# Optimization experiments

Hardware: AMD Instinct MI355X
Metric: run time of the kernel (lower is better)

## Reference

```python
import jax, jax.numpy as jnp
import numpy as np

N = 100000
E = 6400000
NT_DIM = 8
HID = 32


def setup_inputs() -> dict:
    key = jax.random.key(0)
    k1, k2, k3, k4, k5, k6, k7 = jax.random.split(key, 7)
    nt_emb = jax.random.normal(k1, (N, NT_DIM), dtype=jnp.float32)
    edge_index = jax.random.randint(k2, (2, E), 0, N, dtype=jnp.int64)
    lm_mask = jax.random.uniform(k3, (N,), dtype=jnp.float32)
    fan_in1 = 2 * NT_DIM + 2
    lim1 = 1.0 / np.sqrt(fan_in1)
    W1 = jax.random.uniform(k4, (fan_in1, HID), minval=-lim1, maxval=lim1, dtype=jnp.float32)
    b1 = jax.random.uniform(k5, (HID,), minval=-lim1, maxval=lim1, dtype=jnp.float32)
    lim2 = 1.0 / np.sqrt(HID)
    W2 = jax.random.uniform(k6, (HID, 1), minval=-lim2, maxval=lim2, dtype=jnp.float32)
    b2 = jax.random.uniform(k7, (1,), minval=-lim2, maxval=lim2, dtype=jnp.float32)
    return {"nt_emb": nt_emb, "edge_index": edge_index, "lm_mask": lm_mask,
            "W1": W1, "b1": b1, "W2": W2, "b2": b2}


def reference(nt_emb, edge_index, lm_mask, W1, b1, W2, b2):
    s, d = edge_index[0], edge_index[1]
    # [E, 2*nt_dim + 2] edge features: src emb, dst emb, src mask, dst mask
    feat = jnp.concatenate(
        [nt_emb[s], nt_emb[d], lm_mask[s][:, None], lm_mask[d][:, None]], axis=-1)
    h = jax.nn.relu(feat @ W1 + b1)          # [E, hid]
    out = jax.nn.sigmoid(h @ W2 + b2)        # [E, 1]
    return out[:, 0]                         # [E]
```

## Files before the change

### kernel.cpp

```cpp
#include <hip/hip_runtime.h>
#include <hip/hip_bf16.h>

typedef short short8 __attribute__((ext_vector_type(8)));
typedef float floatx4 __attribute__((ext_vector_type(4)));
typedef float floatx16 __attribute__((ext_vector_type(16)));

#define HID 32
#define NTD 8
#define FAN_IN 18

__device__ __forceinline__ short f2bf(float f) {
    union { float f; unsigned u; } v; v.f = f;
    unsigned r = v.u + 0x7fffu + ((v.u >> 16) & 1u);
    return (short)(r >> 16);
}

__device__ __forceinline__ float fast_sigmoid(float x) {
    float e = __builtin_amdgcn_exp2f(x * -1.44269504f);
    return __builtin_amdgcn_rcpf(1.0f + e);
}

__global__ void build_table(const float* __restrict__ emb,
                            const float* __restrict__ mask,
                            short* __restrict__ T, int N) {
    int n = blockIdx.x * blockDim.x + threadIdx.x;
    if (n >= N) return;
    const float4* p = (const float4*)(emb + (size_t)n * NTD);
    float4 lo = p[0], hi = p[1];
    short8 a, b;
    a[0] = f2bf(lo.x); a[1] = f2bf(lo.y); a[2] = f2bf(lo.z); a[3] = f2bf(lo.w);
    a[4] = f2bf(hi.x); a[5] = f2bf(hi.y); a[6] = f2bf(hi.z); a[7] = f2bf(hi.w);
    b[0] = f2bf(mask[n]); b[1] = (short)0x3F80;
    b[2] = b[3] = b[4] = b[5] = b[6] = b[7] = 0;
    short8* row = (short8*)(T + (size_t)n * 16);
    row[0] = a; row[1] = b;
}

struct IdxQ { unsigned sA, dA, sB, dB; };

template <int ESZ>
__device__ __forceinline__ IdxQ load_idx(const char* __restrict__ sBase,
                                         const char* __restrict__ dBase,
                                         unsigned grp, unsigned nGroups,
                                         unsigned E, unsigned c) {
    unsigned g = grp < nGroups ? grp : nGroups - 1u;
    unsigned eA = g * 64u + c;
    unsigned eB = eA + 32u;
    if (eA >= E) eA = E - 1u;
    if (eB >= E) eB = E - 1u;
    IdxQ q;
    q.sA = *(const unsigned*)(sBase + eA * (unsigned)ESZ);
    q.dA = *(const unsigned*)(dBase + eA * (unsigned)ESZ);
    q.sB = *(const unsigned*)(sBase + eB * (unsigned)ESZ);
    q.dB = *(const unsigned*)(dBase + eB * (unsigned)ESZ);
    return q;
}

__device__ __forceinline__ short8 g16(const char* __restrict__ Tc, unsigned idx, unsigned hoff) {
    return *(const short8*)(Tc + (idx * 32u + hoff));
}

template <int ESZ>
__device__ void run32(const char* __restrict__ ei,
                      const char* __restrict__ Tc,
                      float* __restrict__ out, unsigned E,
                      short8 as, short8 ad, const float* __restrict__ w2r, float bias2,
                      unsigned waveId, unsigned nWaves, int h, int c, int lane) {
    const unsigned nGroups = (E + 63u) >> 6;
    const char* sBase = ei;
    const char* dBase = ei + (size_t)E * ESZ;
    const unsigned hoff = (unsigned)h * 16u;

    if (waveId >= nGroups) return;

    unsigned cur = waveId;
    const unsigned stride2 = 2u * nWaves;

    IdxQ i0 = load_idx<ESZ>(sBase, dBase, cur, nGroups, E, (unsigned)c);
    short8 bsA = g16(Tc, i0.sA, hoff);
    short8 bdA = g16(Tc, i0.dA, hoff);
    short8 bsB = g16(Tc, i0.sB, hoff);
    short8 bdB = g16(Tc, i0.dB, hoff);
    IdxQ i1 = load_idx<ESZ>(sBase, dBase, cur + nWaves, nGroups, E, (unsigned)c);

    while (true) {
        short8 nsA = g16(Tc, i1.sA, hoff);
        short8 ndA = g16(Tc, i1.dA, hoff);
        short8 nsB = g16(Tc, i1.sB, hoff);
        short8 ndB = g16(Tc, i1.dB, hoff);
        IdxQ i2 = load_idx<ESZ>(sBase, dBase, cur + stride2, nGroups, E, (unsigned)c);

        floatx16 accA = {0.f,0.f,0.f,0.f,0.f,0.f,0.f,0.f,0.f,0.f,0.f,0.f,0.f,0.f,0.f,0.f};
        floatx16 accB = accA;
        accA = __builtin_amdgcn_mfma_f32_32x32x16_bf16(as, bsA, accA, 0, 0, 0);
        accB = __builtin_amdgcn_mfma_f32_32x32x16_bf16(as, bsB, accB, 0, 0, 0);
        accA = __builtin_amdgcn_mfma_f32_32x32x16_bf16(ad, bdA, accA, 0, 0, 0);
        accB = __builtin_amdgcn_mfma_f32_32x32x16_bf16(ad, bdB, accB, 0, 0, 0);

        float pA0 = 0.f, pA1 = 0.f, pB0 = 0.f, pB1 = 0.f;
        #pragma unroll
        for (int q = 0; q < 16; q += 2) {
            pA0 += fmaxf(accA[q],     0.f) * w2r[q];
            pA1 += fmaxf(accA[q + 1], 0.f) * w2r[q + 1];
            pB0 += fmaxf(accB[q],     0.f) * w2r[q];
            pB1 += fmaxf(accB[q + 1], 0.f) * w2r[q + 1];
        }
        float pA = pA0 + pA1;
        float pB = pB0 + pB1;
        pA += __shfl_xor(pA, 32, 64);
        pB += __shfl_xor(pB, 32, 64);
        float vA = fast_sigmoid(pA + bias2);
        float vB = fast_sigmoid(pB + bias2);

        float v = (h == 0) ? vA : vB;
        unsigned base = cur << 6;
        unsigned e = base + (unsigned)lane;
        if (base + 64u <= E) {
            out[e] = v;
        } else if (e < E) {
            out[e] = v;
        }

        cur += nWaves;
        if (cur >= nGroups) break;
        bsA = nsA; bdA = ndA; bsB = nsB; bdB = ndB;
        i1 = i2;
    }
}

__global__ __launch_bounds__(256, 4) void lg_table_kernel(
    const char* __restrict__ ei_bytes,
    const short* __restrict__ T,
    const float* __restrict__ W1,
    const float* __restrict__ b1,
    const float* __restrict__ W2,
    const float* __restrict__ b2,
    float* __restrict__ out,
    long long E)
{
    const int lane = threadIdx.x & 63;
    const int waveInBlock = threadIdx.x >> 6;
    const unsigned waveId = (unsigned)(blockIdx.x * (blockDim.x >> 6) + waveInBlock);
    const unsigned nWaves = (unsigned)(gridDim.x * (blockDim.x >> 6));

    const int* ei32 = (const int*)ei_bytes;
    int probe = ei32[2 * lane + 1];
    unsigned long long nz = __ballot(probe != 0);
    const int esz = (nz == 0ull) ? 8 : 4;

    const int c = lane & 31;
    const int h = lane >> 5;

    short8 as, ad;
    #pragma unroll
    for (int j = 0; j < 8; ++j) {
        float vs = 0.f, vd = 0.f;
        if (h == 0) {
            vs = W1[j * HID + c];
            vd = W1[(8 + j) * HID + c];
        } else {
            if (j == 0) { vs = W1[16 * HID + c]; vd = W1[17 * HID + c]; }
            else if (j == 1) { vs = b1[c]; }
        }
        as[j] = f2bf(vs);
        ad[j] = f2bf(vd);
    }

    float w2r[16];
    #pragma unroll
    for (int q = 0; q < 16; ++q)
        w2r[q] = W2[(q & 3) + 8 * (q >> 2) + 4 * h];

    const float bias2 = b2[0];

    if (esz == 8)
        run32<8>(ei_bytes, (const char*)T, out, (unsigned)E, as, ad, w2r, bias2,
                 waveId, nWaves, h, c, lane);
    else
        run32<4>(ei_bytes, (const char*)T, out, (unsigned)E, as, ad, w2r, bias2,
                 waveId, nWaves, h, c, lane);
}

__global__ __launch_bounds__(256, 4) void lg_kernel(
    const float* __restrict__ nt_emb,
    const char* __restrict__ ei_bytes,
    const float* __restrict__ lm_mask,
    const float* __restrict__ W1,
    const float* __restrict__ b1,
    const float* __restrict__ W2,
    const float* __restrict__ b2,
    float* __restrict__ out,
    long long E)
{
    const int lane = threadIdx.x & 63;
    const int waveInBlock = threadIdx.x >> 6;
    const long long waveId = (long long)blockIdx.x * (blockDim.x >> 6) + waveInBlock;
    const long long nWaves = (long long)gridDim.x * (blockDim.x >> 6);

    const int* ei32 = (const int*)ei_bytes;
    int probe = ei32[2 * lane + 1];
    unsigned long long nz = __ballot(probe != 0);
    const long long esz = (nz == 0ull) ? 8 : 4;

    const int r = lane & 15;
    const int g = lane >> 4;

    short8 a0, a1;
    #pragma unroll
    for (int j = 0; j < 8; ++j) {
        int k = g * 8 + j;
        float v0 = 0.f, v1 = 0.f;
        if (k < FAN_IN)       { v0 = W1[k * HID + r];      v1 = W1[k * HID + 16 + r]; }
        else if (k == FAN_IN) { v0 = b1[r];                v1 = b1[16 + r]; }
        a0[j] = f2bf(v0);
        a1[j] = f2bf(v1);
    }

    float w2v0[4], w2v1[4];
    #pragma unroll
    for (int q = 0; q < 4; ++q) {
        w2v0[q] = W2[g * 4 + q];
        w2v1[q] = W2[16 + g * 4 + q];
    }
    const float bias2 = b2[0];

    const long long nGroups = (E + 15) >> 4;
    for (long long grp = waveId; grp < nGroups; grp += nWaves) {
        long long e = (grp << 4) + r;
        const bool valid = (e < E);
        long long ec = valid ? e : (E - 1);

        int s = *(const int*)(ei_bytes + ec * esz);
        int d = *(const int*)(ei_bytes + (E + ec) * esz);

        short8 fb;
        #pragma unroll
        for (int j = 0; j < 8; ++j) fb[j] = 0;
        if (g < 2) {
            const float4* p = (const float4*)(nt_emb + (long long)(g == 0 ? s : d) * NTD);
            float4 lo = p[0];
            float4 hi = p[1];
            fb[0] = f2bf(lo.x); fb[1] = f2bf(lo.y); fb[2] = f2bf(lo.z); fb[3] = f2bf(lo.w);
            fb[4] = f2bf(hi.x); fb[5] = f2bf(hi.y); fb[6] = f2bf(hi.z); fb[7] = f2bf(hi.w);
        } else if (g == 2) {
            fb[0] = f2bf(lm_mask[s]);
            fb[1] = f2bf(lm_mask[d]);
            fb[2] = (short)0x3F80;
        }

        floatx4 acc0 = {0.f, 0.f, 0.f, 0.f};
        floatx4 acc1 = {0.f, 0.f, 0.f, 0.f};
        acc0 = __builtin_amdgcn_mfma_f32_16x16x32_bf16(a0, fb, acc0, 0, 0, 0);
        acc1 = __builtin_amdgcn_mfma_f32_16x16x32_bf16(a1, fb, acc1, 0, 0, 0);

        float partial = 0.f;
        #pragma unroll
        for (int q = 0; q < 4; ++q) {
            partial += fmaxf(acc0[q], 0.f) * w2v0[q];
            partial += fmaxf(acc1[q], 0.f) * w2v1[q];
        }
        partial += __shfl_xor(partial, 16, 64);
        partial += __shfl_xor(partial, 32, 64);

        float val = fast_sigmoid(partial + bias2);
        if (g == 0 && valid) out[e] = val;
    }
}

extern "C" void kernel_launch(void* const* d_in, const int* in_sizes, int n_in,
                              void* d_out, int out_size, void* d_ws, size_t ws_size,
                              hipStream_t stream) {
    const float* nt_emb = (const float*)d_in[0];
    const char*  ei     = (const char*)d_in[1];
    const float* lm     = (const float*)d_in[2];
    const float* W1     = (const float*)d_in[3];
    const float* b1     = (const float*)d_in[4];
    const float* W2     = (const float*)d_in[5];
    const float* b2     = (const float*)d_in[6];
    float* out = (float*)d_out;

    long long E = (long long)in_sizes[1] / 2;
    int N = in_sizes[2];

    size_t tableBytes = (size_t)N * 32;
    if (ws_size >= tableBytes) {
        short* T = (short*)d_ws;
        build_table<<<dim3((N + 255) / 256), dim3(256), 0, stream>>>(nt_emb, lm, T, N);
        lg_table_kernel<<<dim3(2048), dim3(256), 0, stream>>>(ei, T, W1, b1, W2, b2, out, E);
    } else {
        lg_kernel<<<dim3(2048), dim3(256), 0, stream>>>(nt_emb, ei, lm, W1, b1, W2, b2, out, E);
    }
}
```

Measured before the change: 77.24 us.

## Deepen index prefetch, use nontemporal loads and stores, raise occupancy hint

Edge-index loads and output stores now use nontemporal builtins, so streaming data is meant to stay out of the cache and leave room for the gathered embedding table. The index prefetch pipeline goes one iteration deeper, adding a third in-flight index set. The tail-store branch is simplified to a single bounds check. The launch bounds minimum blocks per CU rises from 4 to 6, which limits registers per thread and risks spills given the extra prefetch registers.

```diff
diff --git a/kernel.cpp b/kernel.cpp
--- a/kernel.cpp
+++ b/kernel.cpp
@@ -49,10 +49,10 @@
     if (eA >= E) eA = E - 1u;
     if (eB >= E) eB = E - 1u;
     IdxQ q;
-    q.sA = *(const unsigned*)(sBase + eA * (unsigned)ESZ);
-    q.dA = *(const unsigned*)(dBase + eA * (unsigned)ESZ);
-    q.sB = *(const unsigned*)(sBase + eB * (unsigned)ESZ);
-    q.dB = *(const unsigned*)(dBase + eB * (unsigned)ESZ);
+    q.sA = __builtin_nontemporal_load((const unsigned*)(sBase + (size_t)eA * ESZ));
+    q.dA = __builtin_nontemporal_load((const unsigned*)(dBase + (size_t)eA * ESZ));
+    q.sB = __builtin_nontemporal_load((const unsigned*)(sBase + (size_t)eB * ESZ));
+    q.dB = __builtin_nontemporal_load((const unsigned*)(dBase + (size_t)eB * ESZ));
     return q;
 }
 
@@ -74,21 +74,21 @@
     if (waveId >= nGroups) return;
 
     unsigned cur = waveId;
-    const unsigned stride2 = 2u * nWaves;
 
     IdxQ i0 = load_idx<ESZ>(sBase, dBase, cur, nGroups, E, (unsigned)c);
     short8 bsA = g16(Tc, i0.sA, hoff);
     short8 bdA = g16(Tc, i0.dA, hoff);
     short8 bsB = g16(Tc, i0.sB, hoff);
     short8 bdB = g16(Tc, i0.dB, hoff);
-    IdxQ i1 = load_idx<ESZ>(sBase, dBase, cur + nWaves, nGroups, E, (unsigned)c);
+    IdxQ iN1 = load_idx<ESZ>(sBase, dBase, cur + nWaves, nGroups, E, (unsigned)c);
+    IdxQ iN2 = load_idx<ESZ>(sBase, dBase, cur + 2u * nWaves, nGroups, E, (unsigned)c);
 
     while (true) {
-        short8 nsA = g16(Tc, i1.sA, hoff);
-        short8 ndA = g16(Tc, i1.dA, hoff);
-        short8 nsB = g16(Tc, i1.sB, hoff);
-        short8 ndB = g16(Tc, i1.dB, hoff);
-        IdxQ i2 = load_idx<ESZ>(sBase, dBase, cur + stride2, nGroups, E, (unsigned)c);
+        short8 nsA = g16(Tc, iN1.sA, hoff);
+        short8 ndA = g16(Tc, iN1.dA, hoff);
+        short8 nsB = g16(Tc, iN1.sB, hoff);
+        short8 ndB = g16(Tc, iN1.dB, hoff);
+        IdxQ iN3 = load_idx<ESZ>(sBase, dBase, cur + 3u * nWaves, nGroups, E, (unsigned)c);
 
         floatx16 accA = {0.f,0.f,0.f,0.f,0.f,0.f,0.f,0.f,0.f,0.f,0.f,0.f,0.f,0.f,0.f,0.f};
         floatx16 accB = accA;
@@ -113,22 +113,18 @@
         float vB = fast_sigmoid(pB + bias2);
 
         float v = (h == 0) ? vA : vB;
-        unsigned base = cur << 6;
-        unsigned e = base + (unsigned)lane;
-        if (base + 64u <= E) {
-            out[e] = v;
-        } else if (e < E) {
-            out[e] = v;
-        }
+        unsigned e = (cur << 6) + (unsigned)lane;
+        if (e < E) __builtin_nontemporal_store(v, out + e);
 
         cur += nWaves;
         if (cur >= nGroups) break;
         bsA = nsA; bdA = ndA; bsB = nsB; bdB = ndB;
-        i1 = i2;
-    }
-}
-
-__global__ __launch_bounds__(256, 4) void lg_table_kernel(
+        iN1 = iN2;
+        iN2 = iN3;
+    }
+}
+
+__global__ __launch_bounds__(256, 6) void lg_table_kernel(
     const char* __restrict__ ei_bytes,
     const short* __restrict__ T,
     const float* __restrict__ W1,
```

After: 100.6 us. +30.3%, slower.
